# Kernel tuning notes

Measured on AMD Instinct MI355X. Metric: run time of the kernel, lower is better.

The kernel has to match this reference:

```python
import jax, jax.numpy as jnp
import numpy as np

N, E, F, H, L, G = 100000, 1600000, 32, 64, 4, 256
EPS = 1e-5


def setup_inputs() -> dict:
    key = jax.random.key(0)
    ks = jax.random.split(key, 12)
    x = jax.random.normal(ks[0], (N, F), dtype=jnp.float32)
    edge_index = jax.random.randint(ks[1], (2, E), 0, N, dtype=jnp.int32)
    batch = jnp.sort(jax.random.randint(ks[2], (N,), 0, G, dtype=jnp.int32))
    s = 0.1
    return {
        "x": x,
        "edge_index": edge_index,
        "batch": batch,
        "w_embed": jax.random.normal(ks[3], (F, H), dtype=jnp.float32) * s,
        "b_embed": jnp.zeros((H,), dtype=jnp.float32),
        "conv_W": jax.random.normal(ks[4], (L, H, H), dtype=jnp.float32) * s,
        "conv_b": jnp.zeros((L, H), dtype=jnp.float32),
        "bn_gamma": jnp.ones((L, H), dtype=jnp.float32),
        "bn_beta": jnp.zeros((L, H), dtype=jnp.float32),
        "w1": jax.random.normal(ks[5], (H, H // 2), dtype=jnp.float32) * s,
        "b1": jnp.zeros((H // 2,), dtype=jnp.float32),
        "w2": jax.random.normal(ks[6], (H // 2, 1), dtype=jnp.float32) * s,
        "b2": jnp.zeros((1,), dtype=jnp.float32),
    }


def _gcn_conv(h, src, dst, W, b):
    # PyG GCNConv: add self loops, symmetric D^-1/2 (A+I) D^-1/2 normalization
    hw = h @ W  # [N,H]
    deg = jax.ops.segment_sum(jnp.ones((E,), h.dtype), dst, num_segments=N) + 1.0
    dinv = jax.lax.rsqrt(deg)  # [N]
    msg = hw[src] * (dinv[src] * dinv[dst])[:, None]  # [E,H] gather + scale
    agg = jax.ops.segment_sum(msg, dst, num_segments=N)  # scatter-add
    agg = agg + hw * (dinv * dinv)[:, None]  # self-loop contribution
    return agg + b


def _batchnorm(h, gamma, beta):
    # training-mode BatchNorm1d over the node dimension
    mean = jnp.mean(h, axis=0)
    var = jnp.var(h, axis=0)
    return (h - mean) * jax.lax.rsqrt(var + EPS) * gamma + beta


def reference(x, edge_index, batch, w_embed, b_embed, conv_W, conv_b,
              bn_gamma, bn_beta, w1, b1, w2, b2):
    src, dst = edge_index[0], edge_index[1]
    h = x @ w_embed + b_embed  # node embedding [N,H]
    for i in range(L):
        identity = h
        h = _gcn_conv(h, src, dst, conv_W[i], conv_b[i])
        h = _batchnorm(h, bn_gamma[i], bn_beta[i])
        h = jax.nn.relu(h)
        # dropout is identity in eval mode
        h = h + identity  # use_residual=True
    # global mean pool over graphs
    sums = jax.ops.segment_sum(h, batch, num_segments=G)  # [G,H]
    counts = jax.ops.segment_sum(jnp.ones((N,), h.dtype), batch, num_segments=G)
    pooled = sums / jnp.maximum(counts, 1.0)[:, None]
    out = jax.nn.relu(pooled @ w1 + b1)
    out = out @ w2 + b2  # [G,1]
    return out
```

## Files before the change

### kernel.cpp

```cpp
#include <hip/hip_runtime.h>
#include <hip/hip_fp16.h>

#define Nn 100000
#define Ne 1600000
#define Fi 32
#define Hd 64
#define Ll 4
#define Gg 256
#define BN_EPS 1e-5f
#define NPB 128
#define NBINS ((Nn + NPB - 1) / NPB)
#define CHUNK 4096
#define NBLK ((Ne + CHUNK - 1) / CHUNK)
#define IDXW (NBINS + 2)
#define TPAD 68
#define XPAD 36
#define NGB ((Nn + 63) / 64)
#define NSH 128


__global__ void k_scanA(const int* __restrict__ deg, int* __restrict__ row_off,
                        int* __restrict__ bsum) {
    __shared__ int s[256];
    int t = threadIdx.x;
    int i = blockIdx.x * 256 + t;
    int v = (i < Nn) ? deg[i] : 0;
    s[t] = v;
    __syncthreads();
    int x = v;
    for (int off = 1; off < 256; off <<= 1) {
        int u = (t >= off) ? s[t - off] : 0;
        __syncthreads();
        x += u;
        s[t] = x;
        __syncthreads();
    }
    if (i < Nn) row_off[i] = x - v;
    if (t == 255) bsum[blockIdx.x] = x;
}

__global__ void k_scanBG(int* __restrict__ bsum, int nblk,
                         const int* __restrict__ batch, int* __restrict__ gstart) {
    int t = threadIdx.x;
    if (blockIdx.x == 1) {
        if (t < Gg) {
            int lo = 0, hi = Nn;
            while (lo < hi) {
                int mid = (lo + hi) >> 1;
                if (batch[mid] < t) lo = mid + 1; else hi = mid;
            }
            gstart[t] = lo;
            if (t == 0) gstart[Gg] = Nn;
        }
        return;
    }
    __shared__ int s[512];
    int v = (t < nblk) ? bsum[t] : 0;
    s[t] = v;
    __syncthreads();
    int x = v;
    for (int off = 1; off < 512; off <<= 1) {
        int u = (t >= off) ? s[t - off] : 0;
        __syncthreads();
        x += u;
        s[t] = x;
        __syncthreads();
    }
    if (t < nblk) bsum[t] = x - v;
}

__global__ void k_scanC(int* __restrict__ row_off, const int* __restrict__ bsum,
                        const int* __restrict__ deg, float* __restrict__ dinv) {
    int i = blockIdx.x * 256 + threadIdx.x;
    if (i < Nn) {
        row_off[i] += bsum[blockIdx.x];
        dinv[i] = rsqrtf((float)deg[i] + 1.0f);
    }
    if (i == 0) row_off[Nn] = Ne;
}

__global__ __launch_bounds__(256) void k_part(const int* __restrict__ src,
                                              const int* __restrict__ dst,
                                              unsigned* __restrict__ tpack,
                                              unsigned short* __restrict__ idx16) {
    __shared__ int hist[NBINS];
    __shared__ int lofs[NBINS + 1];
    __shared__ int wsum[256];
    __shared__ unsigned stage[CHUNK];
    int blk = blockIdx.x, t = threadIdx.x;
    int e0 = blk * CHUNK;
    int nval = min(CHUNK, Ne - e0);

    for (int i = t; i < NBINS; i += 256) hist[i] = 0;
    __syncthreads();
    for (int i = t; i < nval; i += 256)
        atomicAdd(&hist[dst[e0 + i] >> 7], 1);
    __syncthreads();

    int base = t * 4;
    int loc[4];
    int s = 0;
#pragma unroll
    for (int k = 0; k < 4; k++) {
        int b = base + k;
        int c = (b < NBINS) ? hist[b] : 0;
        loc[k] = s;
        s += c;
    }
    wsum[t] = s;
    __syncthreads();
    int x = s;
    for (int off = 1; off < 256; off <<= 1) {
        int u = (t >= off) ? wsum[t - off] : 0;
        __syncthreads();
        x += u;
        wsum[t] = x;
        __syncthreads();
    }
    int excl = x - s;
#pragma unroll
    for (int k = 0; k < 4; k++) {
        int b = base + k;
        if (b < NBINS) lofs[b] = excl + loc[k];
    }
    if (t == 0) lofs[NBINS] = nval;
    __syncthreads();

    for (int i = t; i <= NBINS; i += 256)
        idx16[(size_t)blk * IDXW + i] = (unsigned short)lofs[i];

    for (int i = t; i < NBINS; i += 256) hist[i] = lofs[i];
    __syncthreads();
    for (int i = t; i < nval; i += 256) {
        int d = dst[e0 + i];
        int sv = src[e0 + i];
        int p = atomicAdd(&hist[d >> 7], 1);
        stage[p] = (unsigned)sv | ((unsigned)(d & (NPB - 1)) << 17);
    }
    __syncthreads();
    for (int i = t; i < nval; i += 256)
        tpack[(size_t)blk * CHUNK + i] = stage[i];
}

__global__ __launch_bounds__(256) void k_deg2(const unsigned* __restrict__ tpack,
                                              const unsigned short* __restrict__ idx16,
                                              int* __restrict__ deg) {
    __shared__ int cnt[NPB];
    int b = blockIdx.x, t = threadIdx.x;
    if (t < NPB) cnt[t] = 0;
    __syncthreads();
    for (int r = t; r < NBLK; r += 256) {
        const unsigned short* row = idx16 + (size_t)r * IDXW;
        int s = row[b], e = row[b + 1];
        const unsigned* tp = tpack + (size_t)r * CHUNK;
        for (int k = s; k < e; k++)
            atomicAdd(&cnt[tp[k] >> 17], 1);
    }
    __syncthreads();
    int node = b * NPB + t;
    if (t < NPB && node < Nn) deg[node] = cnt[t];
}

__global__ __launch_bounds__(256) void k_csr(const int* __restrict__ row_off,
                                             const unsigned* __restrict__ tpack,
                                             const unsigned short* __restrict__ idx16,
                                             int* __restrict__ esrc) {
    __shared__ int cur[NPB];
    int b = blockIdx.x, t = threadIdx.x;
    int n0 = b * NPB;
    int e0 = row_off[n0];
    if (t < NPB) {
        int node = n0 + t;
        cur[t] = (node < Nn) ? (row_off[node] - e0) : 0;
    }
    __syncthreads();
    for (int r = t; r < NBLK; r += 256) {
        const unsigned short* row = idx16 + (size_t)r * IDXW;
        int s = row[b], e = row[b + 1];
        const unsigned* tp = tpack + (size_t)r * CHUNK;
        for (int k = s; k < e; k++) {
            unsigned v = tp[k];
            int p = atomicAdd(&cur[v >> 17], 1);
            esrc[e0 + p] = (int)(v & 0x1FFFFu);
        }
    }
}


#define MT_FMA(AV, W0, W1, W2, W3, R)                                          \
    acc[R][0] = fmaf(AV.x, W0.x, acc[R][0]);                                   \
    acc[R][0] = fmaf(AV.y, W1.x, acc[R][0]);                                   \
    acc[R][0] = fmaf(AV.z, W2.x, acc[R][0]);                                   \
    acc[R][0] = fmaf(AV.w, W3.x, acc[R][0]);                                   \
    acc[R][1] = fmaf(AV.x, W0.y, acc[R][1]);                                   \
    acc[R][1] = fmaf(AV.y, W1.y, acc[R][1]);                                   \
    acc[R][1] = fmaf(AV.z, W2.y, acc[R][1]);                                   \
    acc[R][1] = fmaf(AV.w, W3.y, acc[R][1]);                                   \
    acc[R][2] = fmaf(AV.x, W0.z, acc[R][2]);                                   \
    acc[R][2] = fmaf(AV.y, W1.z, acc[R][2]);                                   \
    acc[R][2] = fmaf(AV.z, W2.z, acc[R][2]);                                   \
    acc[R][2] = fmaf(AV.w, W3.z, acc[R][2]);                                   \
    acc[R][3] = fmaf(AV.x, W0.w, acc[R][3]);                                   \
    acc[R][3] = fmaf(AV.y, W1.w, acc[R][3]);                                   \
    acc[R][3] = fmaf(AV.z, W2.w, acc[R][3]);                                   \
    acc[R][3] = fmaf(AV.w, W3.w, acc[R][3]);

__device__ inline void store_half4(unsigned short* dst, float a, float b,
                                   float c, float d) {
    __half2 p0 = __floats2half2_rn(a, b);
    __half2 p1 = __floats2half2_rn(c, d);
    uint2 u;
    u.x = *(unsigned*)&p0;
    u.y = *(unsigned*)&p1;
    *(uint2*)dst = u;
}

__global__ __launch_bounds__(256, 4) void k_gemmF2(const float* __restrict__ agg,
                                                   const float* __restrict__ bnsc,
                                                   const float* __restrict__ bnsh,
                                                   float* __restrict__ h,
                                                   const float* __restrict__ W,
                                                   const float* __restrict__ dinv,
                                                   unsigned short* __restrict__ hwh) {
    __shared__ float hs[64 * TPAD];
    __shared__ float ws[64 * 64];
    int t = threadIdx.x;
    int n0 = blockIdx.x * 64;

    for (int f = t; f < 1024; f += 256)
        ((float4*)ws)[f] = ((const float4*)W)[f];

    for (int f = t; f < 1024; f += 256) {
        int row = f >> 4, c4 = (f & 15) * 4;
        int node = n0 + row;
        if (node < Nn) {
            float4 a  = *(const float4*)(agg + (size_t)node * Hd + c4);
            float4 ho = *(const float4*)(h + (size_t)node * Hd + c4);
            float4 sc = ((const float4*)bnsc)[f & 15];
            float4 sh = ((const float4*)bnsh)[f & 15];
            float4 r4;
            r4.x = fmaxf(fmaf(a.x, sc.x, sh.x), 0.f) + ho.x;
            r4.y = fmaxf(fmaf(a.y, sc.y, sh.y), 0.f) + ho.y;
            r4.z = fmaxf(fmaf(a.z, sc.z, sh.z), 0.f) + ho.z;
            r4.w = fmaxf(fmaf(a.w, sc.w, sh.w), 0.f) + ho.w;
            *(float4*)(h + (size_t)node * Hd + c4) = r4;
            *(float4*)&hs[row * TPAD + c4] = r4;
        } else {
            *(float4*)&hs[row * TPAD + c4] = make_float4(0.f, 0.f, 0.f, 0.f);
        }
    }
    __syncthreads();

    int i = t >> 4, j = t & 15;
    float acc[4][4] = {};
#pragma unroll 2
    for (int k = 0; k < 64; k += 4) {
        float4 w0 = *(const float4*)&ws[(k + 0) * 64 + 4 * j];
        float4 w1 = *(const float4*)&ws[(k + 1) * 64 + 4 * j];
        float4 w2 = *(const float4*)&ws[(k + 2) * 64 + 4 * j];
        float4 w3 = *(const float4*)&ws[(k + 3) * 64 + 4 * j];
        float4 a0 = *(const float4*)&hs[(4 * i + 0) * TPAD + k];
        float4 a1 = *(const float4*)&hs[(4 * i + 1) * TPAD + k];
        float4 a2 = *(const float4*)&hs[(4 * i + 2) * TPAD + k];
        float4 a3 = *(const float4*)&hs[(4 * i + 3) * TPAD + k];
        MT_FMA(a0, w0, w1, w2, w3, 0)
        MT_FMA(a1, w0, w1, w2, w3, 1)
        MT_FMA(a2, w0, w1, w2, w3, 2)
        MT_FMA(a3, w0, w1, w2, w3, 3)
    }
#pragma unroll
    for (int r = 0; r < 4; r++) {
        int node = n0 + 4 * i + r;
        if (node < Nn) {
            float dv = dinv[node];
            store_half4(hwh + (size_t)node * Hd + 4 * j,
                        acc[r][0] * dv, acc[r][1] * dv, acc[r][2] * dv,
                        acc[r][3] * dv);
        }
    }
}

__global__ __launch_bounds__(256, 4) void k_embed_gemm2(const float* __restrict__ x,
                                                        const float* __restrict__ we,
                                                        const float* __restrict__ be,
                                                        const float* __restrict__ W,
                                                        float* __restrict__ h,
                                                        const float* __restrict__ dinv,
                                                        unsigned short* __restrict__ hwh) {
    __shared__ float uni[64 * XPAD + 32 * 64];
    __shared__ float hs[64 * TPAD];
    __shared__ float bes[64];
    float* xs  = uni;
    float* wes = uni + 64 * XPAD;
    float* ws  = uni;
    int t = threadIdx.x;
    int n0 = blockIdx.x * 64;

    for (int f = t; f < 512; f += 256)
        ((float4*)wes)[f] = ((const float4*)we)[f];
    if (t < 64) bes[t] = be[t];

    for (int f = t; f < 512; f += 256) {
        int row = f >> 3, c4 = (f & 7) * 4;
        int node = n0 + row;
        float4 v = (node < Nn) ? *(const float4*)(x + (size_t)node * Fi + c4)
                               : make_float4(0.f, 0.f, 0.f, 0.f);
        *(float4*)&xs[row * XPAD + c4] = v;
    }
    __syncthreads();

    int i = t >> 4, j = t & 15;
    {
        float acc[4][4];
#pragma unroll
        for (int r = 0; r < 4; r++)
#pragma unroll
            for (int c = 0; c < 4; c++) acc[r][c] = bes[4 * j + c];
#pragma unroll 2
        for (int k = 0; k < 32; k += 4) {
            float4 w0 = *(const float4*)&wes[(k + 0) * 64 + 4 * j];
            float4 w1 = *(const float4*)&wes[(k + 1) * 64 + 4 * j];
            float4 w2 = *(const float4*)&wes[(k + 2) * 64 + 4 * j];
            float4 w3 = *(const float4*)&wes[(k + 3) * 64 + 4 * j];
            float4 a0 = *(const float4*)&xs[(4 * i + 0) * XPAD + k];
            float4 a1 = *(const float4*)&xs[(4 * i + 1) * XPAD + k];
            float4 a2 = *(const float4*)&xs[(4 * i + 2) * XPAD + k];
            float4 a3 = *(const float4*)&xs[(4 * i + 3) * XPAD + k];
            MT_FMA(a0, w0, w1, w2, w3, 0)
            MT_FMA(a1, w0, w1, w2, w3, 1)
            MT_FMA(a2, w0, w1, w2, w3, 2)
            MT_FMA(a3, w0, w1, w2, w3, 3)
        }
#pragma unroll
        for (int r = 0; r < 4; r++) {
            int node = n0 + 4 * i + r;
            float4 hv = make_float4(acc[r][0], acc[r][1], acc[r][2], acc[r][3]);
            *(float4*)&hs[(4 * i + r) * TPAD + 4 * j] = hv;
            if (node < Nn)
                *(float4*)(h + (size_t)node * Hd + 4 * j) = hv;
        }
    }
    __syncthreads();
    for (int f = t; f < 1024; f += 256)
        ((float4*)ws)[f] = ((const float4*)W)[f];
    __syncthreads();
    {
        float acc[4][4] = {};
#pragma unroll 2
        for (int k = 0; k < 64; k += 4) {
            float4 w0 = *(const float4*)&ws[(k + 0) * 64 + 4 * j];
            float4 w1 = *(const float4*)&ws[(k + 1) * 64 + 4 * j];
            float4 w2 = *(const float4*)&ws[(k + 2) * 64 + 4 * j];
            float4 w3 = *(const float4*)&ws[(k + 3) * 64 + 4 * j];
            float4 a0 = *(const float4*)&hs[(4 * i + 0) * TPAD + k];
            float4 a1 = *(const float4*)&hs[(4 * i + 1) * TPAD + k];
            float4 a2 = *(const float4*)&hs[(4 * i + 2) * TPAD + k];
            float4 a3 = *(const float4*)&hs[(4 * i + 3) * TPAD + k];
            MT_FMA(a0, w0, w1, w2, w3, 0)
            MT_FMA(a1, w0, w1, w2, w3, 1)
            MT_FMA(a2, w0, w1, w2, w3, 2)
            MT_FMA(a3, w0, w1, w2, w3, 3)
        }
#pragma unroll
        for (int r = 0; r < 4; r++) {
            int node = n0 + 4 * i + r;
            if (node < Nn) {
                float dv = dinv[node];
                store_half4(hwh + (size_t)node * Hd + 4 * j,
                            acc[r][0] * dv, acc[r][1] * dv, acc[r][2] * dv,
                            acc[r][3] * dv);
            }
        }
    }
}


__global__ __launch_bounds__(256) void k_gatherH(const unsigned short* __restrict__ hwh,
                                                 const float* __restrict__ dinv,
                                                 const int* __restrict__ row_off,
                                                 const int* __restrict__ esrc,
                                                 const float* __restrict__ bias,
                                                 float* __restrict__ agg,
                                                 float* __restrict__ bnacc) {
    int g = threadIdx.x >> 3;
    int l = threadIdx.x & 7;
    int node = blockIdx.x * 32 + g;
    float di = dinv[node];
    float acc[8];

    uint4 v = *(const uint4*)(hwh + (size_t)node * Hd + l * 8);
#pragma unroll
    for (int q = 0; q < 4; q++) {
        float2 f = __half22float2(*(__half2*)(((unsigned*)&v) + q));
        acc[2 * q]     = f.x;
        acc[2 * q + 1] = f.y;
    }

    int e = row_off[node], e1 = row_off[node + 1];
    for (; e + 7 < e1; e += 8) {
        uint4 vv[8];
#pragma unroll
        for (int u = 0; u < 8; u++)
            vv[u] = *(const uint4*)(hwh + (size_t)esrc[e + u] * Hd + l * 8);
#pragma unroll
        for (int u = 0; u < 8; u++) {
#pragma unroll
            for (int q = 0; q < 4; q++) {
                float2 f = __half22float2(*(__half2*)(((unsigned*)&vv[u]) + q));
                acc[2 * q]     += f.x;
                acc[2 * q + 1] += f.y;
            }
        }
    }
    for (; e + 1 < e1; e += 2) {
        uint4 v0 = *(const uint4*)(hwh + (size_t)esrc[e] * Hd + l * 8);
        uint4 v1 = *(const uint4*)(hwh + (size_t)esrc[e + 1] * Hd + l * 8);
#pragma unroll
        for (int q = 0; q < 4; q++) {
            float2 f0 = __half22float2(*(__half2*)(((unsigned*)&v0) + q));
            float2 f1 = __half22float2(*(__half2*)(((unsigned*)&v1) + q));
            acc[2 * q]     += f0.x + f1.x;
            acc[2 * q + 1] += f0.y + f1.y;
        }
    }
    if (e < e1) {
        uint4 v0 = *(const uint4*)(hwh + (size_t)esrc[e] * Hd + l * 8);
#pragma unroll
        for (int q = 0; q < 4; q++) {
            float2 f0 = __half22float2(*(__half2*)(((unsigned*)&v0) + q));
            acc[2 * q]     += f0.x;
            acc[2 * q + 1] += f0.y;
        }
    }

#pragma unroll
    for (int q = 0; q < 8; q++)
        acc[q] = fmaf(acc[q], di, bias[l * 8 + q]);

    *(float4*)(agg + (size_t)node * Hd + l * 8)     = make_float4(acc[0], acc[1], acc[2], acc[3]);
    *(float4*)(agg + (size_t)node * Hd + l * 8 + 4) = make_float4(acc[4], acc[5], acc[6], acc[7]);

    __shared__ float ls[2048];
    *(float4*)&ls[g * 64 + l * 8]     = make_float4(acc[0], acc[1], acc[2], acc[3]);
    *(float4*)&ls[g * 64 + l * 8 + 4] = make_float4(acc[4], acc[5], acc[6], acc[7]);
    __syncthreads();
    int t = threadIdx.x;
    if (t < 64) {
        float s = 0.f, s2 = 0.f;
#pragma unroll
        for (int gg = 0; gg < 32; gg++) {
            float vv = ls[gg * 64 + t];
            s += vv;
            s2 = fmaf(vv, vv, s2);
        }
        float* a = bnacc + (blockIdx.x & (NSH - 1)) * 128;
        atomicAdd(&a[t], s);
        atomicAdd(&a[64 + t], s2);
    }
}

__global__ void k_bnfinal(const float* __restrict__ acc, const float* __restrict__ gamma,
                          const float* __restrict__ beta, float* __restrict__ bnsc,
                          float* __restrict__ bnsh) {
    int c = threadIdx.x;
    if (c >= 64) return;
    float s = 0.f, s2 = 0.f;
    for (int sh = 0; sh < NSH; sh++) {
        s  += acc[sh * 128 + c];
        s2 += acc[sh * 128 + 64 + c];
    }
    float mean = s / (float)Nn;
    float var = s2 / (float)Nn - mean * mean;
    var = fmaxf(var, 0.f);
    float sc = gamma[c] * rsqrtf(var + BN_EPS);
    bnsc[c] = sc;
    bnsh[c] = beta[c] - mean * sc;
}

__global__ __launch_bounds__(1024) void k_poolF(const float* __restrict__ agg,
                                                const float* __restrict__ bnsc,
                                                const float* __restrict__ bnsh,
                                                const float* __restrict__ h,
                                                const int* __restrict__ gstart,
                                                float* __restrict__ pooled) {
    int g = blockIdx.x;
    int t = threadIdx.x;
    int ch = t & 63, sl = t >> 6;
    float sc = bnsc[ch], shv = bnsh[ch];
    int n0 = gstart[g], n1 = gstart[g + 1];
    float s = 0.f;
    for (int n = n0 + sl; n < n1; n += 16) {
        float a  = agg[(size_t)n * Hd + ch];
        float ho = h[(size_t)n * Hd + ch];
        s += fmaxf(fmaf(a, sc, shv), 0.f) + ho;
    }
    __shared__ float ls[1024];
    ls[t] = s;
    __syncthreads();
    if (t < 64) {
        float acc = 0.f;
#pragma unroll
        for (int k = 0; k < 16; k++) acc += ls[k * 64 + t];
        float cnt = (float)(n1 - n0);
        pooled[g * Hd + t] = acc / fmaxf(cnt, 1.0f);
    }
}

__global__ __launch_bounds__(256) void k_head(const float* __restrict__ pooled,
                                              const float* __restrict__ w1,
                                              const float* __restrict__ b1,
                                              const float* __restrict__ w2,
                                              const float* __restrict__ b2,
                                              float* __restrict__ out) {
    __shared__ float sw1[Hd * 32], sw2[32], sb1[32];
    int t = threadIdx.x;
    for (int i = t; i < Hd * 32; i += 256) sw1[i] = w1[i];
    if (t < 32) { sw2[t] = w2[t]; sb1[t] = b1[t]; }
    __syncthreads();
    float acc2[32];
#pragma unroll
    for (int k = 0; k < 32; k++) acc2[k] = sb1[k];
    for (int j = 0; j < Hd; j++) {
        float pj = pooled[t * Hd + j];
#pragma unroll
        for (int k = 0; k < 32; k++) acc2[k] = fmaf(pj, sw1[j * 32 + k], acc2[k]);
    }
    float o = b2[0];
#pragma unroll
    for (int k = 0; k < 32; k++) o += fmaxf(acc2[k], 0.f) * sw2[k];
    out[t] = o;
}


extern "C" void kernel_launch(void* const* d_in, const int* in_sizes, int n_in,
                              void* d_out, int out_size, void* d_ws, size_t ws_size,
                              hipStream_t stream) {
    const float* x       = (const float*)d_in[0];
    const int*   eidx    = (const int*)d_in[1];
    const int*   batch   = (const int*)d_in[2];
    const float* w_embed = (const float*)d_in[3];
    const float* b_embed = (const float*)d_in[4];
    const float* conv_W  = (const float*)d_in[5];
    const float* conv_b  = (const float*)d_in[6];
    const float* gamma   = (const float*)d_in[7];
    const float* beta    = (const float*)d_in[8];
    const float* w1      = (const float*)d_in[9];
    const float* b1      = (const float*)d_in[10];
    const float* w2      = (const float*)d_in[11];
    const float* b2      = (const float*)d_in[12];
    const int* src = eidx;
    const int* dst = eidx + Ne;

    char* p = (char*)d_ws;
    auto alloc = [&](size_t bytes) -> void* {
        void* r = (void*)p;
        p += (bytes + 255) / 256 * 256;
        return r;
    };
    float*    h       = (float*)alloc((size_t)Nn * Hd * 4);
    unsigned short* hwh = (unsigned short*)alloc((size_t)Nn * Hd * 2);
    float*    agg     = (float*)alloc((size_t)Nn * Hd * 4);
    int*      deg     = (int*)alloc((size_t)Nn * 4);
    int*      row_off = (int*)alloc((size_t)(Nn + 1) * 4);
    float*    dinv    = (float*)alloc((size_t)Nn * 4);
    int*      bsum    = (int*)alloc(512 * 4);
    int*      esrc    = (int*)alloc((size_t)Ne * 4);
    unsigned* tpack   = (unsigned*)alloc((size_t)NBLK * CHUNK * 4);
    unsigned short* idx16 = (unsigned short*)alloc((size_t)NBLK * IDXW * 2);
    float*    bnacc   = (float*)alloc((size_t)Ll * NSH * 128 * 4);
    float*    bnsc    = (float*)alloc(64 * 4);
    float*    bnsh    = (float*)alloc(64 * 4);
    float*    pooled  = (float*)alloc((size_t)Gg * Hd * 4);
    int*      gstart  = (int*)alloc((size_t)(Gg + 1) * 4);
    (void)ws_size; (void)in_sizes; (void)n_in; (void)out_size;

    const int NB_N = (Nn + 255) / 256;
    const int NB_G32 = Nn / 32;

    hipMemsetAsync(bnacc, 0, (size_t)Ll * NSH * 128 * 4, stream);

    k_part<<<NBLK, 256, 0, stream>>>(src, dst, tpack, idx16);
    k_deg2<<<NBINS, 256, 0, stream>>>(tpack, idx16, deg);
    k_scanA<<<NB_N, 256, 0, stream>>>(deg, row_off, bsum);
    k_scanBG<<<2, 512, 0, stream>>>(bsum, NB_N, batch, gstart);
    k_scanC<<<NB_N, 256, 0, stream>>>(row_off, bsum, deg, dinv);
    k_csr<<<NBINS, 256, 0, stream>>>(row_off, tpack, idx16, esrc);

    k_embed_gemm2<<<NGB, 256, 0, stream>>>(x, w_embed, b_embed, conv_W, h, dinv, hwh);

    for (int i = 0; i < Ll; i++) {
        if (i > 0)
            k_gemmF2<<<NGB, 256, 0, stream>>>(agg, bnsc, bnsh, h,
                                              conv_W + (size_t)i * Hd * Hd, dinv, hwh);
        k_gatherH<<<NB_G32, 256, 0, stream>>>(hwh, dinv, row_off, esrc,
                                              conv_b + (size_t)i * Hd, agg,
                                              bnacc + (size_t)i * NSH * 128);
        k_bnfinal<<<1, 64, 0, stream>>>(bnacc + (size_t)i * NSH * 128,
                                        gamma + (size_t)i * Hd,
                                        beta + (size_t)i * Hd, bnsc, bnsh);
    }

    k_poolF<<<Gg, 1024, 0, stream>>>(agg, bnsc, bnsh, h, gstart, pooled);
    k_head<<<1, 256, 0, stream>>>(pooled, w1, b1, w2, b2, (float*)d_out);
}
```

Baseline: 342.6 us.

## Fuse BN finalize into consumers and stage edge indices in LDS per wave

Removes the single-block k_bnfinal launch by having every k_gemmF2 and k_poolF block reduce the sharded BN sums and compute scale/shift into shared memory. The gather kernel now has each wavefront cooperatively load its contiguous range of CSR source indices into LDS in 256-entry windows, then reads neighbour indices from LDS instead of issuing per-lane global loads. This cuts launch overhead and redundant index traffic, at the cost of redundant 128-shard reductions in every block and an extra LDS round-trip per window.

Measured after the change: 346.4 us. No clear change (+1.1%).

```diff
diff --git a/kernel.cpp b/kernel.cpp
--- a/kernel.cpp
+++ b/kernel.cpp
@@ -17,6 +17,7 @@
 #define XPAD 36
 #define NGB ((Nn + 63) / 64)
 #define NSH 128
+#define WSZ 256
 
 
 __global__ void k_scanA(const int* __restrict__ deg, int* __restrict__ row_off,
@@ -216,19 +217,35 @@
 }
 
 __global__ __launch_bounds__(256, 4) void k_gemmF2(const float* __restrict__ agg,
-                                                   const float* __restrict__ bnsc,
-                                                   const float* __restrict__ bnsh,
+                                                   const float* __restrict__ bnacc,
+                                                   const float* __restrict__ gamma,
+                                                   const float* __restrict__ beta,
                                                    float* __restrict__ h,
                                                    const float* __restrict__ W,
                                                    const float* __restrict__ dinv,
                                                    unsigned short* __restrict__ hwh) {
     __shared__ float hs[64 * TPAD];
     __shared__ float ws[64 * 64];
+    __shared__ float bsc[64], bsh[64];
     int t = threadIdx.x;
     int n0 = blockIdx.x * 64;
 
     for (int f = t; f < 1024; f += 256)
         ((float4*)ws)[f] = ((const float4*)W)[f];
+
+    if (t < 64) {
+        float s = 0.f, s2 = 0.f;
+        for (int shd = 0; shd < NSH; shd++) {
+            s  += bnacc[shd * 128 + t];
+            s2 += bnacc[shd * 128 + 64 + t];
+        }
+        float mean = s / (float)Nn;
+        float var = fmaxf(s2 / (float)Nn - mean * mean, 0.f);
+        float scv = gamma[t] * rsqrtf(var + BN_EPS);
+        bsc[t] = scv;
+        bsh[t] = beta[t] - mean * scv;
+    }
+    __syncthreads();
 
     for (int f = t; f < 1024; f += 256) {
         int row = f >> 4, c4 = (f & 15) * 4;
@@ -236,8 +253,8 @@
         if (node < Nn) {
             float4 a  = *(const float4*)(agg + (size_t)node * Hd + c4);
             float4 ho = *(const float4*)(h + (size_t)node * Hd + c4);
-            float4 sc = ((const float4*)bnsc)[f & 15];
-            float4 sh = ((const float4*)bnsh)[f & 15];
+            float4 sc = ((const float4*)bsc)[f & 15];
+            float4 sh = ((const float4*)bsh)[f & 15];
             float4 r4;
             r4.x = fmaxf(fmaf(a.x, sc.x, sh.x), 0.f) + ho.x;
             r4.y = fmaxf(fmaf(a.y, sc.y, sh.y), 0.f) + ho.y;
@@ -382,12 +399,18 @@
                                                  const float* __restrict__ bias,
                                                  float* __restrict__ agg,
                                                  float* __restrict__ bnacc) {
-    int g = threadIdx.x >> 3;
-    int l = threadIdx.x & 7;
-    int node = blockIdx.x * 32 + g;
+    __shared__ int se[4][WSZ];
+    __shared__ float ls[2048];
+    int t = threadIdx.x;
+    int w = t >> 6, lane = t & 63;
+    int g = lane >> 3, l = lane & 7;
+    int node = blockIdx.x * 32 + w * 8 + g;
     float di = dinv[node];
+    int en0 = row_off[node], en1 = row_off[node + 1];
+    int we0 = __shfl(en0, 0, 64);
+    int we1 = __shfl(en1, 63, 64);
+
     float acc[8];
-
     uint4 v = *(const uint4*)(hwh + (size_t)node * Hd + l * 8);
 #pragma unroll
     for (int q = 0; q < 4; q++) {
@@ -396,41 +419,39 @@
         acc[2 * q + 1] = f.y;
     }
 
-    int e = row_off[node], e1 = row_off[node + 1];
-    for (; e + 7 < e1; e += 8) {
-        uint4 vv[8];
-#pragma unroll
-        for (int u = 0; u < 8; u++)
-            vv[u] = *(const uint4*)(hwh + (size_t)esrc[e + u] * Hd + l * 8);
-#pragma unroll
-        for (int u = 0; u < 8; u++) {
+    for (int wb = we0; wb < we1; wb += WSZ) {
+        int cnt = min(WSZ, we1 - wb);
+        for (int k2 = lane; k2 < cnt; k2 += 64)
+            se[w][k2] = esrc[wb + k2];
+        __builtin_amdgcn_wave_barrier();
+        asm volatile("s_waitcnt lgkmcnt(0)" ::: "memory");
+        int j  = max(en0, wb) - wb;
+        int j1 = min(en1, wb + cnt) - wb;
+        for (; j + 7 < j1; j += 8) {
+            uint4 vv[8];
+#pragma unroll
+            for (int u = 0; u < 8; u++)
+                vv[u] = *(const uint4*)(hwh + (size_t)se[w][j + u] * Hd + l * 8);
+#pragma unroll
+            for (int u = 0; u < 8; u++) {
+#pragma unroll
+                for (int q = 0; q < 4; q++) {
+                    float2 f = __half22float2(*(__half2*)(((unsigned*)&vv[u]) + q));
+                    acc[2 * q]     += f.x;
+                    acc[2 * q + 1] += f.y;
+                }
+            }
+        }
+        for (; j < j1; j++) {
+            uint4 v0 = *(const uint4*)(hwh + (size_t)se[w][j] * Hd + l * 8);
 #pragma unroll
             for (int q = 0; q < 4; q++) {
-                float2 f = __half22float2(*(__half2*)(((unsigned*)&vv[u]) + q));
+                float2 f = __half22float2(*(__half2*)(((unsigned*)&v0) + q));
                 acc[2 * q]     += f.x;
                 acc[2 * q + 1] += f.y;
             }
         }
-    }
-    for (; e + 1 < e1; e += 2) {
-        uint4 v0 = *(const uint4*)(hwh + (size_t)esrc[e] * Hd + l * 8);
-        uint4 v1 = *(const uint4*)(hwh + (size_t)esrc[e + 1] * Hd + l * 8);
-#pragma unroll
-        for (int q = 0; q < 4; q++) {
-            float2 f0 = __half22float2(*(__half2*)(((unsigned*)&v0) + q));
-            float2 f1 = __half22float2(*(__half2*)(((unsigned*)&v1) + q));
-            acc[2 * q]     += f0.x + f1.x;
-            acc[2 * q + 1] += f0.y + f1.y;
-        }
-    }
-    if (e < e1) {
-        uint4 v0 = *(const uint4*)(hwh + (size_t)esrc[e] * Hd + l * 8);
-#pragma unroll
-        for (int q = 0; q < 4; q++) {
-            float2 f0 = __half22float2(*(__half2*)(((unsigned*)&v0) + q));
-            acc[2 * q]     += f0.x;
-            acc[2 * q + 1] += f0.y;
-        }
+        __builtin_amdgcn_wave_barrier();
     }
 
 #pragma unroll
@@ -440,11 +461,10 @@
     *(float4*)(agg + (size_t)node * Hd + l * 8)     = make_float4(acc[0], acc[1], acc[2], acc[3]);
     *(float4*)(agg + (size_t)node * Hd + l * 8 + 4) = make_float4(acc[4], acc[5], acc[6], acc[7]);
 
-    __shared__ float ls[2048];
-    *(float4*)&ls[g * 64 + l * 8]     = make_float4(acc[0], acc[1], acc[2], acc[3]);
-    *(float4*)&ls[g * 64 + l * 8 + 4] = make_float4(acc[4], acc[5], acc[6], acc[7]);
-    __syncthreads();
-    int t = threadIdx.x;
+    int g32 = t >> 3;
+    *(float4*)&ls[g32 * 64 + l * 8]     = make_float4(acc[0], acc[1], acc[2], acc[3]);
+    *(float4*)&ls[g32 * 64 + l * 8 + 4] = make_float4(acc[4], acc[5], acc[6], acc[7]);
+    __syncthreads();
     if (t < 64) {
         float s = 0.f, s2 = 0.f;
 #pragma unroll
@@ -459,34 +479,32 @@
     }
 }
 
-__global__ void k_bnfinal(const float* __restrict__ acc, const float* __restrict__ gamma,
-                          const float* __restrict__ beta, float* __restrict__ bnsc,
-                          float* __restrict__ bnsh) {
-    int c = threadIdx.x;
-    if (c >= 64) return;
-    float s = 0.f, s2 = 0.f;
-    for (int sh = 0; sh < NSH; sh++) {
-        s  += acc[sh * 128 + c];
-        s2 += acc[sh * 128 + 64 + c];
-    }
-    float mean = s / (float)Nn;
-    float var = s2 / (float)Nn - mean * mean;
-    var = fmaxf(var, 0.f);
-    float sc = gamma[c] * rsqrtf(var + BN_EPS);
-    bnsc[c] = sc;
-    bnsh[c] = beta[c] - mean * sc;
-}
-
 __global__ __launch_bounds__(1024) void k_poolF(const float* __restrict__ agg,
-                                                const float* __restrict__ bnsc,
-                                                const float* __restrict__ bnsh,
+                                                const float* __restrict__ bnacc,
+                                                const float* __restrict__ gamma,
+                                                const float* __restrict__ beta,
                                                 const float* __restrict__ h,
                                                 const int* __restrict__ gstart,
                                                 float* __restrict__ pooled) {
+    __shared__ float ls[1024];
+    __shared__ float bsc[64], bsh[64];
     int g = blockIdx.x;
     int t = threadIdx.x;
+    if (t < 64) {
+        float s = 0.f, s2 = 0.f;
+        for (int shd = 0; shd < NSH; shd++) {
+            s  += bnacc[shd * 128 + t];
+            s2 += bnacc[shd * 128 + 64 + t];
+        }
+        float mean = s / (float)Nn;
+        float var = fmaxf(s2 / (float)Nn - mean * mean, 0.f);
+        float scv = gamma[t] * rsqrtf(var + BN_EPS);
+        bsc[t] = scv;
+        bsh[t] = beta[t] - mean * scv;
+    }
+    __syncthreads();
     int ch = t & 63, sl = t >> 6;
-    float sc = bnsc[ch], shv = bnsh[ch];
+    float sc = bsc[ch], shv = bsh[ch];
     int n0 = gstart[g], n1 = gstart[g + 1];
     float s = 0.f;
     for (int n = n0 + sl; n < n1; n += 16) {
@@ -494,7 +512,6 @@
         float ho = h[(size_t)n * Hd + ch];
         s += fmaxf(fmaf(a, sc, shv), 0.f) + ho;
     }
-    __shared__ float ls[1024];
     ls[t] = s;
     __syncthreads();
     if (t < 64) {
@@ -568,8 +585,6 @@
     unsigned* tpack   = (unsigned*)alloc((size_t)NBLK * CHUNK * 4);
     unsigned short* idx16 = (unsigned short*)alloc((size_t)NBLK * IDXW * 2);
     float*    bnacc   = (float*)alloc((size_t)Ll * NSH * 128 * 4);
-    float*    bnsc    = (float*)alloc(64 * 4);
-    float*    bnsh    = (float*)alloc(64 * 4);
     float*    pooled  = (float*)alloc((size_t)Gg * Hd * 4);
     int*      gstart  = (int*)alloc((size_t)(Gg + 1) * 4);
     (void)ws_size; (void)in_sizes; (void)n_in; (void)out_size;
@@ -590,16 +605,17 @@
 
     for (int i = 0; i < Ll; i++) {
         if (i > 0)
-            k_gemmF2<<<NGB, 256, 0, stream>>>(agg, bnsc, bnsh, h,
+            k_gemmF2<<<NGB, 256, 0, stream>>>(agg, bnacc + (size_t)(i - 1) * NSH * 128,
+                                              gamma + (size_t)(i - 1) * Hd,
+                                              beta + (size_t)(i - 1) * Hd, h,
                                               conv_W + (size_t)i * Hd * Hd, dinv, hwh);
         k_gatherH<<<NB_G32, 256, 0, stream>>>(hwh, dinv, row_off, esrc,
                                               conv_b + (size_t)i * Hd, agg,
                                               bnacc + (size_t)i * NSH * 128);
-        k_bnfinal<<<1, 64, 0, stream>>>(bnacc + (size_t)i * NSH * 128,
-                                        gamma + (size_t)i * Hd,
-                                        beta + (size_t)i * Hd, bnsc, bnsh);
-    }
-
-    k_poolF<<<Gg, 1024, 0, stream>>>(agg, bnsc, bnsh, h, gstart, pooled);
+    }
+
+    k_poolF<<<Gg, 1024, 0, stream>>>(agg, bnacc + (size_t)(Ll - 1) * NSH * 128,
+                                     gamma + (size_t)(Ll - 1) * Hd,
+                                     beta + (size_t)(Ll - 1) * Hd, h, gstart, pooled);
     k_head<<<1, 256, 0, stream>>>(pooled, w1, b1, w2, b2, (float*)d_out);
 }
```
